# Kernel optimization log

Measured on AMD Instinct MI355X. Metric: run time of the kernel, lower is better.

The kernel has to match this reference:

```python
import jax, jax.numpy as jnp
import numpy as np
from jax import lax

IOU_THRESHOLD = 0.5
TOP = 1000


def setup_inputs() -> dict:
    key = jax.random.key(0)
    k1, k2, k3, k4, k5 = jax.random.split(key, 5)
    B, P = 16, 20000
    # valid (x1, y1, x2, y2) boxes on an ~800x800 image
    x1 = jax.random.uniform(k1, (B, P)) * 800.0
    y1 = jax.random.uniform(k2, (B, P)) * 800.0
    w = jax.random.uniform(k3, (B, P)) * 200.0 + 1.0
    h = jax.random.uniform(k4, (B, P)) * 200.0 + 1.0
    reg = jnp.stack([x1, y1, x1 + w, y1 + h], axis=-1)  # [B, P, 4]
    cls = jax.random.normal(k5, (B, P))                  # [B, P]
    return {"reg": reg, "cls": cls}


def _pairwise_iou(boxes):
    """boxes: [B, N, 4] (x1,y1,x2,y2) -> IoU [B, N, N]."""
    a = boxes[:, :, None, :]  # [B, N, 1, 4]
    b = boxes[:, None, :, :]  # [B, 1, N, 4]
    xx1 = jnp.maximum(a[..., 0], b[..., 0])
    yy1 = jnp.maximum(a[..., 1], b[..., 1])
    xx2 = jnp.minimum(a[..., 2], b[..., 2])
    yy2 = jnp.minimum(a[..., 3], b[..., 3])
    inter = jnp.clip(xx2 - xx1, 0.0) * jnp.clip(yy2 - yy1, 0.0)
    area_a = (a[..., 2] - a[..., 0]) * (a[..., 3] - a[..., 1])
    area_b = (b[..., 2] - b[..., 0]) * (b[..., 3] - b[..., 1])
    return inter / (area_a + area_b - inter)


def reference(reg, cls):
    B = cls.shape[0]
    # sort by confidence descending, gather boxes, keep top
    order = jnp.argsort(-cls, axis=1)                      # [B, P]
    sorted_cls = jnp.take_along_axis(cls, order, axis=1)[:, :TOP]            # [B, N]
    sorted_reg = jnp.take_along_axis(reg, order[:, :, None], axis=1)[:, :TOP]  # [B, N, 4]
    N = sorted_cls.shape[1]

    iou = _pairwise_iou(sorted_reg)                        # [B, N, N]

    # sequential greedy suppression: if box i still kept, drop boxes with IoU>=thr
    def body(mask, i):
        keep_i = mask[:, i]                                # [B]
        tmp = iou[:, i, :] < IOU_THRESHOLD                 # [B, N]
        upd = (mask & tmp).at[:, i].set(True)
        new_mask = jnp.where(keep_i[:, None], upd, mask)
        return new_mask, None

    mask0 = jnp.ones((B, N), dtype=bool)
    mask, _ = lax.scan(body, mask0, jnp.arange(N))

    out_reg = jnp.where(mask[:, :, None], sorted_reg, 0.0)
    out_cls = jnp.where(mask, sorted_cls, 0.0)
    return out_reg, out_cls
```

## Files before the change

kernel.cpp:

```cpp
#include <hip/hip_runtime.h>
#include <stdint.h>

#define BATCH 16
#define NPTS  20000
#define TOPK  1000
#define NKPT  20
#define NBIN  2048
#define NCOPY 4
#define CANDCAP 2048

__device__ __forceinline__ uint32_t key_desc(float f) {
    uint32_t u = __float_as_uint(f);
    uint32_t m = (u & 0x80000000u) ? ~u : (u | 0x80000000u);
    return ~m;
}

__device__ __forceinline__ float key_undo(uint32_t k) {
    uint32_t m = ~k;
    uint32_t u = (m & 0x80000000u) ? (m & 0x7FFFFFFFu) : ~m;
    return __uint_as_float(u);
}

__device__ __forceinline__ void hist_scan_find(
    uint32_t (*wh)[NBIN], uint32_t* wsum, uint32_t* wpre,
    int* sh_T, int* sh_r, int* sh_binc,
    int tid, int wave, int lane, uint32_t r)
{
    uint32_t m0 = 0, m1 = 0;
    #pragma unroll
    for (int cpy = 0; cpy < NCOPY; ++cpy) { m0 += wh[cpy][2*tid]; m1 += wh[cpy][2*tid+1]; }
    uint32_t s = m0 + m1, x = s;
    #pragma unroll
    for (int d = 1; d < 64; d <<= 1) { uint32_t t = __shfl_up(x, d); if (lane >= d) x += t; }
    if (lane == 63) wsum[wave] = x;
    __syncthreads();
    if (wave == 0 && lane < 16) {
        uint32_t v = wsum[lane], y = v;
        #pragma unroll
        for (int d = 1; d < 16; d <<= 1) { uint32_t t = __shfl_up(y, d); if (lane >= d) y += t; }
        wpre[lane] = y - v;
    }
    __syncthreads();
    uint32_t e = wpre[wave] + (x - s);
    if (r >= e && r < e + s) {
        if (r < e + m0) { *sh_T = 2*tid;     *sh_r = (int)(r - e);      *sh_binc = (int)m0; }
        else            { *sh_T = 2*tid + 1; *sh_r = (int)(r - e - m0); *sh_binc = (int)m1; }
    }
}

__device__ __forceinline__ void push64(bool pred, uint64_t val, int* cntr,
                                       uint64_t* list, int lane) {
    uint64_t mask = __ballot(pred);
    if (mask) {
        int first = __ffsll((long long)mask) - 1;
        int base = 0;
        if (lane == first) base = atomicAdd(cntr, (int)__popcll(mask));
        base = __shfl(base, first);
        if (pred) {
            int off = (int)__popcll(mask & ((1ull << lane) - 1ull));
            list[base + off] = val;
        }
    }
}

__device__ __forceinline__ void wave_select(const uint64_t* lst, int n, int r,
                                            uint64_t* out, int wave, int lane) {
    if (wave == 0) {
        uint64_t my = (lane < n) ? lst[lane] : ~0ull;
        int rank = 0;
        for (int i = 0; i < n; ++i) { uint64_t o = __shfl(my, i); if (o < my) rank++; }
        if (lane < n && rank == r) *out = my;
    }
}

__device__ uint64_t bit_search(const uint32_t* klds, uint64_t known, uint64_t kmask,
                               int startbit, uint32_t r, int* sh_c,
                               int tid, int lane) {
    for (int bit = startbit; bit >= 0; --bit) {
        if (tid == 0) *sh_c = 0;
        __syncthreads();
        uint32_t local = 0;
        #pragma unroll
        for (int j = 0; j < NKPT; ++j) {
            int p = tid + j * 1024;
            if (p < NPTS) {
                uint64_t k64 = ((uint64_t)klds[p] << 32) | (uint32_t)p;
                if ((k64 & kmask) == known && !((k64 >> bit) & 1ull)) local++;
            }
        }
        #pragma unroll
        for (int d = 1; d < 64; d <<= 1) local += __shfl_xor(local, d);
        if (lane == 0 && local) atomicAdd(sh_c, (int)local);
        __syncthreads();
        uint32_t c0 = (uint32_t)*sh_c;
        if (r >= c0) { known |= 1ull << bit; r -= c0; }
        kmask |= 1ull << bit;
        __syncthreads();
    }
    return known;
}

__global__ __launch_bounds__(1024) void topk_kernel(
    const float* __restrict__ reg, const float* __restrict__ cls,
    float4* __restrict__ ws_boxes, float* __restrict__ ws_cls)
{
    __shared__ uint32_t klds[NPTS];
    __shared__ uint32_t whist[NCOPY][NBIN];
    __shared__ uint32_t wsum[16], wpre[16];
    __shared__ int      sh_T, sh_r, sh_binc, sh_cnt;
    __shared__ uint64_t sh_kthkey;
    __shared__ uint64_t cand[CANDCAP];
    __shared__ uint64_t cand2[64];
    __shared__ uint64_t sel[1024];

    const int b = blockIdx.x, tid = threadIdx.x;
    const int wave = tid >> 6, lane = tid & 63;
    const float* c = cls + (size_t)b * NPTS;

    #pragma unroll
    for (int i = 0; i < NCOPY * NBIN / 1024; ++i) ((uint32_t*)whist)[tid + i * 1024] = 0;
    #pragma unroll
    for (int j = 0; j < NKPT; ++j) {
        int p = tid + j * 1024;
        if (p < NPTS) klds[p] = key_desc(c[p]);
    }
    __syncthreads();

    #pragma unroll
    for (int j = 0; j < NKPT; ++j) {
        int p = tid + j * 1024;
        if (p < NPTS) atomicAdd(&whist[wave >> 2][klds[p] >> 21], 1u);
    }
    __syncthreads();
    hist_scan_find(whist, wsum, wpre, &sh_T, &sh_r, &sh_binc, tid, wave, lane, TOPK - 1);
    __syncthreads();
    const int T1 = sh_T; int r = sh_r; const int cnt1 = sh_binc;
    uint64_t known = (uint64_t)(uint32_t)T1 << 53;

    if (cnt1 <= 64) {
        if (tid == 0) sh_cnt = 0;
        __syncthreads();
        #pragma unroll
        for (int j = 0; j < NKPT; ++j) {
            int p = tid + j * 1024;
            uint32_t k = (p < NPTS) ? klds[p] : 0xFFFFFFFFu;
            push64(p < NPTS && (k >> 21) == (uint32_t)T1,
                   ((uint64_t)k << 32) | (uint32_t)p, &sh_cnt, cand2, lane);
        }
        __syncthreads();
        wave_select(cand2, cnt1, r, &sh_kthkey, wave, lane);
        __syncthreads();
    } else if (cnt1 <= CANDCAP) {
        if (tid == 0) sh_cnt = 0;
        __syncthreads();
        #pragma unroll
        for (int j = 0; j < NKPT; ++j) {
            int p = tid + j * 1024;
            uint32_t k = (p < NPTS) ? klds[p] : 0xFFFFFFFFu;
            push64(p < NPTS && (k >> 21) == (uint32_t)T1,
                   ((uint64_t)k << 32) | (uint32_t)p, &sh_cnt, cand, lane);
        }
        __syncthreads();
        #pragma unroll
        for (int i = 0; i < NCOPY * NBIN / 1024; ++i) ((uint32_t*)whist)[tid + i * 1024] = 0;
        __syncthreads();
        for (int i = tid; i < cnt1; i += 1024)
            atomicAdd(&whist[wave >> 2][(uint32_t)((cand[i] >> 42) & 2047)], 1u);
        __syncthreads();
        hist_scan_find(whist, wsum, wpre, &sh_T, &sh_r, &sh_binc, tid, wave, lane, (uint32_t)r);
        __syncthreads();
        const int T2 = sh_T; r = sh_r; const int cnt2 = sh_binc;
        known |= (uint64_t)(uint32_t)T2 << 42;
        if (cnt2 <= 64) {
            if (tid == 0) sh_cnt = 0;
            __syncthreads();
            for (int i = tid; i < cnt1; i += 1024)
                push64(((cand[i] >> 42) & 2047) == (uint64_t)(uint32_t)T2,
                       cand[i], &sh_cnt, cand2, lane);
            __syncthreads();
            wave_select(cand2, cnt2, r, &sh_kthkey, wave, lane);
            __syncthreads();
        } else {
            uint64_t kk = bit_search(klds, known, 0xFFFFFC0000000000ull, 41,
                                     (uint32_t)r, &sh_cnt, tid, lane);
            if (tid == 0) sh_kthkey = kk;
            __syncthreads();
        }
    } else {
        uint64_t kk = bit_search(klds, known, 0xFFE0000000000000ull, 52,
                                 (uint32_t)r, &sh_cnt, tid, lane);
        if (tid == 0) sh_kthkey = kk;
        __syncthreads();
    }
    const uint64_t kthkey = sh_kthkey;

    if (tid == 0) sh_cnt = 0;
    sel[tid] = ~0ull;
    __syncthreads();
    #pragma unroll
    for (int j = 0; j < NKPT; ++j) {
        int p = tid + j * 1024;
        uint64_t key = (p < NPTS) ? (((uint64_t)klds[p] << 32) | (uint32_t)p) : ~0ull;
        push64(key <= kthkey, key, &sh_cnt, sel, lane);
    }
    __syncthreads();

    uint64_t v = sel[tid];
    for (int k = 2; k <= 1024; k <<= 1) {
        for (int j = k >> 1; j >= 64; j >>= 1) {
            __syncthreads();
            sel[tid] = v;
            __syncthreads();
            uint64_t o = sel[tid ^ j];
            bool upper = (tid & j) != 0;
            bool asc   = (tid & k) == 0;
            v = (upper == asc) ? (v > o ? v : o) : (v < o ? v : o);
        }
        int j0 = (k >> 1) < 64 ? (k >> 1) : 32;
        for (int j = j0; j >= 1; j >>= 1) {
            uint64_t o = __shfl_xor(v, j);
            bool upper = (tid & j) != 0;
            bool asc   = (tid & k) == 0;
            v = (upper == asc) ? (v > o ? v : o) : (v < o ? v : o);
        }
    }

    if (tid < TOPK) {
        int p = (int)(v & 0xFFFFFFFFull);
        ws_boxes[b * TOPK + tid] = ((const float4*)reg)[(size_t)b * NPTS + p];
        ws_cls[b * TOPK + tid] = key_undo((uint32_t)(v >> 32));
    }
}

__global__ __launch_bounds__(256) void iou_kernel(
    const float4* __restrict__ ws_boxes, uint32_t* __restrict__ suppT)
{
    __shared__ float4 boxes[TOPK];
    __shared__ float  areas[TOPK];
    const int b     = blockIdx.y;
    const int chunk = blockIdx.x;
    const int tid   = threadIdx.x;
    for (int j = tid; j < TOPK; j += 256) {
        float4 v = ws_boxes[b * TOPK + j];
        boxes[j] = v;
        areas[j] = (v.z - v.x) * (v.w - v.y);
    }
    __syncthreads();

    const int lane = tid & 63;
    const int wave = tid >> 6;
    const int rbeg = chunk * 63;
    const int rend = (rbeg + 63 < TOPK) ? (rbeg + 63) : TOPK;
    uint32_t* t = suppT + (size_t)b * 32 * 1024;

    for (int i = rbeg + wave; i < rend; i += 4) {
        float4 a = boxes[i];
        float areaA = areas[i];
        uint64_t mine = 0;
        #pragma unroll
        for (int w = 0; w < 16; ++w) {
            int col = (w << 6) | lane;
            bool sup = false;
            if (col < TOPK) {
                float4 bb = boxes[col];
                float xx1 = fmaxf(a.x, bb.x);
                float yy1 = fmaxf(a.y, bb.y);
                float xx2 = fminf(a.z, bb.z);
                float yy2 = fminf(a.w, bb.w);
                float iw = fmaxf(xx2 - xx1, 0.0f);
                float ih = fmaxf(yy2 - yy1, 0.0f);
                float inter = iw * ih;
                float areaB = areas[col];
                float iou = inter / (areaA + areaB - inter);
                sup = (iou >= 0.5f);
            }
            uint64_t m = __ballot(sup);
            if (lane == w) mine = m;
        }
        if (lane < 16) {
            t[(2 * lane + 0) * 1024 + i] = (uint32_t)(mine & 0xFFFFFFFFull);
            t[(2 * lane + 1) * 1024 + i] = (uint32_t)(mine >> 32);
        }
    }
}

__global__ __launch_bounds__(64) void sweep_kernel(
    const uint32_t* __restrict__ suppT, const float4* __restrict__ ws_boxes,
    const float* __restrict__ ws_cls, float* __restrict__ out)
{
    const int b    = blockIdx.x;
    const int lane = threadIdx.x;
    const int myw  = lane & 31;
    const uint32_t* base = suppT + (size_t)b * 32 * 1024;

    uint32_t remv = 0, keptw = 0;
    uint4 dgA[8], clA[8], dgB[8], clB[8];

#define LOADG(W, DG, CL) { \
    const uint4* dp_ = (const uint4*)(base + (W) * 1024 + (W) * 32); \
    const uint4* cp_ = (const uint4*)(base + myw * 1024 + (W) * 32); \
    _Pragma("unroll") \
    for (int k_ = 0; k_ < 8; ++k_) { DG[k_] = dp_[k_]; CL[k_] = cp_[k_]; } }

#define STEP(D, C, BBIT) { \
    uint32_t live_ = (((~cur) >> (BBIT)) & 1u) & (uint32_t)((BBIT) < nb); \
    uint32_t msk_ = (uint32_t)0 - live_; \
    kmask |= (live_ << (BBIT)); \
    cur  |= (D) & msk_; \
    acc  |= (C) & msk_; }

#define PROC(W, DG, CL) { \
    const int nb = ((W) == 31) ? (TOPK - 31 * 32) : 32; \
    uint32_t cur = __shfl(remv, (W)); \
    uint32_t kmask = 0, acc = 0; \
    _Pragma("unroll") \
    for (int k_ = 0; k_ < 8; ++k_) { \
        STEP(DG[k_].x, CL[k_].x, 4 * k_ + 0); \
        STEP(DG[k_].y, CL[k_].y, 4 * k_ + 1); \
        STEP(DG[k_].z, CL[k_].z, 4 * k_ + 2); \
        STEP(DG[k_].w, CL[k_].w, 4 * k_ + 3); \
    } \
    remv |= acc; \
    if (myw == (W)) keptw = kmask; }

    LOADG(0, dgA, clA);
    #pragma unroll 1
    for (int w2 = 0; w2 < 16; ++w2) {
        const int wE = 2 * w2, wO = 2 * w2 + 1;
        LOADG(wO, dgB, clB);
        PROC(wE, dgA, clA);
        if (wO + 1 < 32) LOADG(wO + 1, dgA, clA);
        PROC(wO, dgB, clB);
    }

    __shared__ uint32_t skept[32];
    if (lane < 32) skept[lane] = keptw;
    __syncthreads();

    const float4* bx = ws_boxes + (size_t)b * TOPK;
    const float*  bc = ws_cls + (size_t)b * TOPK;
    float4* outr = (float4*)out + (size_t)b * TOPK;
    float*  outc = out + (size_t)BATCH * TOPK * 4 + (size_t)b * TOPK;
    for (int j = lane; j < TOPK; j += 64) {
        uint32_t keep = (skept[j >> 5] >> (j & 31)) & 1u;
        float4 v = bx[j];
        float cv = bc[j];
        outr[j] = keep ? v : make_float4(0.f, 0.f, 0.f, 0.f);
        outc[j] = keep ? cv : 0.0f;
    }
#undef LOADG
#undef STEP
#undef PROC
}

extern "C" void kernel_launch(void* const* d_in, const int* in_sizes, int n_in,
                              void* d_out, int out_size, void* d_ws, size_t ws_size,
                              hipStream_t stream) {
    (void)in_sizes; (void)n_in; (void)out_size; (void)ws_size;
    const float* reg = (const float*)d_in[0];
    const float* cls = (const float*)d_in[1];
    float* out = (float*)d_out;
    char* ws = (char*)d_ws;

    float4*   ws_boxes = (float4*)ws;
    float*    ws_cls   = (float*)(ws + 256000);
    uint32_t* suppT    = (uint32_t*)(ws + 320000);

    topk_kernel<<<dim3(BATCH), dim3(1024), 0, stream>>>(reg, cls, ws_boxes, ws_cls);
    iou_kernel<<<dim3(16, BATCH), dim3(256), 0, stream>>>(ws_boxes, suppT);
    sweep_kernel<<<dim3(BATCH), dim3(64), 0, stream>>>(suppT, ws_boxes, ws_cls, out);
}
```

Measured before the change: 74.24 us.

## Use single-level 4096-bin top-k select, rank-count ordering, upper-triangle IoU

The top-k selection now uses one 4096-bin histogram pass instead of a two-level 2048-bin refinement with a candidate buffer. Inputs whose threshold bin holds more than 64 entries fall back to a bit search. The 1024-element bitonic sort, with its many block barriers, is replaced by having each thread count how many selected keys are smaller than its own and scatter to that rank. The IoU kernel now computes only the upper-triangular 64-column words for each row and interleaves rows across blocks to balance the triangular work. Costs: the rank count does 1024 shared reads per thread, and the larger histogram uses more LDS and takes longer to clear and scan.

```diff
diff --git a/kernel.cpp b/kernel.cpp
--- a/kernel.cpp
+++ b/kernel.cpp
@@ -5,9 +5,8 @@
 #define NPTS  20000
 #define TOPK  1000
 #define NKPT  20
-#define NBIN  2048
+#define NBIN  4096
 #define NCOPY 4
-#define CANDCAP 2048
 
 __device__ __forceinline__ uint32_t key_desc(float f) {
     uint32_t u = __float_as_uint(f);
@@ -19,33 +18,6 @@
     uint32_t m = ~k;
     uint32_t u = (m & 0x80000000u) ? (m & 0x7FFFFFFFu) : ~m;
     return __uint_as_float(u);
-}
-
-__device__ __forceinline__ void hist_scan_find(
-    uint32_t (*wh)[NBIN], uint32_t* wsum, uint32_t* wpre,
-    int* sh_T, int* sh_r, int* sh_binc,
-    int tid, int wave, int lane, uint32_t r)
-{
-    uint32_t m0 = 0, m1 = 0;
-    #pragma unroll
-    for (int cpy = 0; cpy < NCOPY; ++cpy) { m0 += wh[cpy][2*tid]; m1 += wh[cpy][2*tid+1]; }
-    uint32_t s = m0 + m1, x = s;
-    #pragma unroll
-    for (int d = 1; d < 64; d <<= 1) { uint32_t t = __shfl_up(x, d); if (lane >= d) x += t; }
-    if (lane == 63) wsum[wave] = x;
-    __syncthreads();
-    if (wave == 0 && lane < 16) {
-        uint32_t v = wsum[lane], y = v;
-        #pragma unroll
-        for (int d = 1; d < 16; d <<= 1) { uint32_t t = __shfl_up(y, d); if (lane >= d) y += t; }
-        wpre[lane] = y - v;
-    }
-    __syncthreads();
-    uint32_t e = wpre[wave] + (x - s);
-    if (r >= e && r < e + s) {
-        if (r < e + m0) { *sh_T = 2*tid;     *sh_r = (int)(r - e);      *sh_binc = (int)m0; }
-        else            { *sh_T = 2*tid + 1; *sh_r = (int)(r - e - m0); *sh_binc = (int)m1; }
-    }
 }
 
 __device__ __forceinline__ void push64(bool pred, uint64_t val, int* cntr,
@@ -106,10 +78,9 @@
 {
     __shared__ uint32_t klds[NPTS];
     __shared__ uint32_t whist[NCOPY][NBIN];
-    __shared__ uint32_t wsum[16], wpre[16];
-    __shared__ int      sh_T, sh_r, sh_binc, sh_cnt;
+    __shared__ uint32_t wsum[16], wpre16[16];
+    __shared__ int      sh_T, sh_r, sh_binc, sh_cnt, sh_c;
     __shared__ uint64_t sh_kthkey;
-    __shared__ uint64_t cand[CANDCAP];
     __shared__ uint64_t cand2[64];
     __shared__ uint64_t sel[1024];
 
@@ -129,13 +100,42 @@
     #pragma unroll
     for (int j = 0; j < NKPT; ++j) {
         int p = tid + j * 1024;
-        if (p < NPTS) atomicAdd(&whist[wave >> 2][klds[p] >> 21], 1u);
-    }
-    __syncthreads();
-    hist_scan_find(whist, wsum, wpre, &sh_T, &sh_r, &sh_binc, tid, wave, lane, TOPK - 1);
-    __syncthreads();
-    const int T1 = sh_T; int r = sh_r; const int cnt1 = sh_binc;
-    uint64_t known = (uint64_t)(uint32_t)T1 << 53;
+        if (p < NPTS) atomicAdd(&whist[wave >> 2][klds[p] >> 20], 1u);
+    }
+    __syncthreads();
+
+    {
+        uint32_t m0 = 0, m1 = 0, m2 = 0, m3 = 0;
+        #pragma unroll
+        for (int cpy = 0; cpy < NCOPY; ++cpy) {
+            m0 += whist[cpy][4 * tid + 0]; m1 += whist[cpy][4 * tid + 1];
+            m2 += whist[cpy][4 * tid + 2]; m3 += whist[cpy][4 * tid + 3];
+        }
+        uint32_t s = m0 + m1 + m2 + m3, x = s;
+        #pragma unroll
+        for (int d = 1; d < 64; d <<= 1) { uint32_t t = __shfl_up(x, d); if (lane >= d) x += t; }
+        if (lane == 63) wsum[wave] = x;
+        __syncthreads();
+        if (wave == 0 && lane < 16) {
+            uint32_t v = wsum[lane], y = v;
+            #pragma unroll
+            for (int d = 1; d < 16; d <<= 1) { uint32_t t = __shfl_up(y, d); if (lane >= d) y += t; }
+            wpre16[lane] = y - v;
+        }
+        __syncthreads();
+        uint32_t E = wpre16[wave] + (x - s);
+        uint32_t r9 = TOPK - 1;
+        if (r9 >= E && r9 < E + s) {
+            uint32_t rr = r9 - E;
+            if      (rr < m0)           { sh_T = 4*tid + 0; sh_r = (int)rr;            sh_binc = (int)m0; }
+            else if (rr < m0+m1)        { sh_T = 4*tid + 1; sh_r = (int)(rr-m0);       sh_binc = (int)m1; }
+            else if (rr < m0+m1+m2)     { sh_T = 4*tid + 2; sh_r = (int)(rr-m0-m1);    sh_binc = (int)m2; }
+            else                        { sh_T = 4*tid + 3; sh_r = (int)(rr-m0-m1-m2); sh_binc = (int)m3; }
+        }
+    }
+    __syncthreads();
+    const uint32_t T1 = (uint32_t)sh_T;
+    const int r = sh_r, cnt1 = sh_binc;
 
     if (cnt1 <= 64) {
         if (tid == 0) sh_cnt = 0;
@@ -144,54 +144,17 @@
         for (int j = 0; j < NKPT; ++j) {
             int p = tid + j * 1024;
             uint32_t k = (p < NPTS) ? klds[p] : 0xFFFFFFFFu;
-            push64(p < NPTS && (k >> 21) == (uint32_t)T1,
+            push64(p < NPTS && (k >> 20) == T1,
                    ((uint64_t)k << 32) | (uint32_t)p, &sh_cnt, cand2, lane);
         }
         __syncthreads();
         wave_select(cand2, cnt1, r, &sh_kthkey, wave, lane);
-        __syncthreads();
-    } else if (cnt1 <= CANDCAP) {
-        if (tid == 0) sh_cnt = 0;
-        __syncthreads();
-        #pragma unroll
-        for (int j = 0; j < NKPT; ++j) {
-            int p = tid + j * 1024;
-            uint32_t k = (p < NPTS) ? klds[p] : 0xFFFFFFFFu;
-            push64(p < NPTS && (k >> 21) == (uint32_t)T1,
-                   ((uint64_t)k << 32) | (uint32_t)p, &sh_cnt, cand, lane);
-        }
-        __syncthreads();
-        #pragma unroll
-        for (int i = 0; i < NCOPY * NBIN / 1024; ++i) ((uint32_t*)whist)[tid + i * 1024] = 0;
-        __syncthreads();
-        for (int i = tid; i < cnt1; i += 1024)
-            atomicAdd(&whist[wave >> 2][(uint32_t)((cand[i] >> 42) & 2047)], 1u);
-        __syncthreads();
-        hist_scan_find(whist, wsum, wpre, &sh_T, &sh_r, &sh_binc, tid, wave, lane, (uint32_t)r);
-        __syncthreads();
-        const int T2 = sh_T; r = sh_r; const int cnt2 = sh_binc;
-        known |= (uint64_t)(uint32_t)T2 << 42;
-        if (cnt2 <= 64) {
-            if (tid == 0) sh_cnt = 0;
-            __syncthreads();
-            for (int i = tid; i < cnt1; i += 1024)
-                push64(((cand[i] >> 42) & 2047) == (uint64_t)(uint32_t)T2,
-                       cand[i], &sh_cnt, cand2, lane);
-            __syncthreads();
-            wave_select(cand2, cnt2, r, &sh_kthkey, wave, lane);
-            __syncthreads();
-        } else {
-            uint64_t kk = bit_search(klds, known, 0xFFFFFC0000000000ull, 41,
-                                     (uint32_t)r, &sh_cnt, tid, lane);
-            if (tid == 0) sh_kthkey = kk;
-            __syncthreads();
-        }
     } else {
-        uint64_t kk = bit_search(klds, known, 0xFFE0000000000000ull, 52,
-                                 (uint32_t)r, &sh_cnt, tid, lane);
+        uint64_t kk = bit_search(klds, (uint64_t)T1 << 52, 0xFFF0000000000000ull,
+                                 51, (uint32_t)r, &sh_c, tid, lane);
         if (tid == 0) sh_kthkey = kk;
-        __syncthreads();
-    }
+    }
+    __syncthreads();
     const uint64_t kthkey = sh_kthkey;
 
     if (tid == 0) sh_cnt = 0;
@@ -205,30 +168,14 @@
     }
     __syncthreads();
 
-    uint64_t v = sel[tid];
-    for (int k = 2; k <= 1024; k <<= 1) {
-        for (int j = k >> 1; j >= 64; j >>= 1) {
-            __syncthreads();
-            sel[tid] = v;
-            __syncthreads();
-            uint64_t o = sel[tid ^ j];
-            bool upper = (tid & j) != 0;
-            bool asc   = (tid & k) == 0;
-            v = (upper == asc) ? (v > o ? v : o) : (v < o ? v : o);
-        }
-        int j0 = (k >> 1) < 64 ? (k >> 1) : 32;
-        for (int j = j0; j >= 1; j >>= 1) {
-            uint64_t o = __shfl_xor(v, j);
-            bool upper = (tid & j) != 0;
-            bool asc   = (tid & k) == 0;
-            v = (upper == asc) ? (v > o ? v : o) : (v < o ? v : o);
-        }
-    }
-
-    if (tid < TOPK) {
-        int p = (int)(v & 0xFFFFFFFFull);
-        ws_boxes[b * TOPK + tid] = ((const float4*)reg)[(size_t)b * NPTS + p];
-        ws_cls[b * TOPK + tid] = key_undo((uint32_t)(v >> 32));
+    uint64_t e = sel[tid];
+    int rk = 0;
+    #pragma unroll 4
+    for (int m2 = 0; m2 < 1024; ++m2) rk += (sel[m2] < e) ? 1 : 0;
+    if (e != ~0ull) {
+        int p = (int)(e & 0xFFFFFFFFull);
+        ws_boxes[b * TOPK + rk] = ((const float4*)reg)[(size_t)b * NPTS + p];
+        ws_cls[b * TOPK + rk] = key_undo((uint32_t)(e >> 32));
     }
 }
 
@@ -237,29 +184,28 @@
 {
     __shared__ float4 boxes[TOPK];
     __shared__ float  areas[TOPK];
-    const int b     = blockIdx.y;
-    const int chunk = blockIdx.x;
-    const int tid   = threadIdx.x;
-    for (int j = tid; j < TOPK; j += 256) {
-        float4 v = ws_boxes[b * TOPK + j];
-        boxes[j] = v;
-        areas[j] = (v.z - v.x) * (v.w - v.y);
+    const int b   = blockIdx.y;
+    const int j   = blockIdx.x;
+    const int tid = threadIdx.x;
+    for (int i = tid; i < TOPK; i += 256) {
+        float4 v = ws_boxes[b * TOPK + i];
+        boxes[i] = v;
+        areas[i] = (v.z - v.x) * (v.w - v.y);
     }
     __syncthreads();
 
     const int lane = tid & 63;
     const int wave = tid >> 6;
-    const int rbeg = chunk * 63;
-    const int rend = (rbeg + 63 < TOPK) ? (rbeg + 63) : TOPK;
     uint32_t* t = suppT + (size_t)b * 32 * 1024;
 
-    for (int i = rbeg + wave; i < rend; i += 4) {
+    for (int k = wave; ; k += 4) {
+        const int i = j + (k << 4);
+        if (i >= TOPK) break;
         float4 a = boxes[i];
         float areaA = areas[i];
         uint64_t mine = 0;
-        #pragma unroll
-        for (int w = 0; w < 16; ++w) {
-            int col = (w << 6) | lane;
+        for (int w2 = i >> 6; w2 < 16; ++w2) {
+            int col = (w2 << 6) | lane;
             bool sup = false;
             if (col < TOPK) {
                 float4 bb = boxes[col];
@@ -270,12 +216,11 @@
                 float iw = fmaxf(xx2 - xx1, 0.0f);
                 float ih = fmaxf(yy2 - yy1, 0.0f);
                 float inter = iw * ih;
-                float areaB = areas[col];
-                float iou = inter / (areaA + areaB - inter);
+                float iou = inter / (areaA + areas[col] - inter);
                 sup = (iou >= 0.5f);
             }
             uint64_t m = __ballot(sup);
-            if (lane == w) mine = m;
+            if (lane == w2) mine = m;
         }
         if (lane < 16) {
             t[(2 * lane + 0) * 1024 + i] = (uint32_t)(mine & 0xFFFFFFFFull);
@@ -341,12 +286,12 @@
     const float*  bc = ws_cls + (size_t)b * TOPK;
     float4* outr = (float4*)out + (size_t)b * TOPK;
     float*  outc = out + (size_t)BATCH * TOPK * 4 + (size_t)b * TOPK;
-    for (int j = lane; j < TOPK; j += 64) {
-        uint32_t keep = (skept[j >> 5] >> (j & 31)) & 1u;
-        float4 v = bx[j];
-        float cv = bc[j];
-        outr[j] = keep ? v : make_float4(0.f, 0.f, 0.f, 0.f);
-        outc[j] = keep ? cv : 0.0f;
+    for (int i = lane; i < TOPK; i += 64) {
+        uint32_t keep = (skept[i >> 5] >> (i & 31)) & 1u;
+        float4 v = bx[i];
+        float cv = bc[i];
+        outr[i] = keep ? v : make_float4(0.f, 0.f, 0.f, 0.f);
+        outc[i] = keep ? cv : 0.0f;
     }
 #undef LOADG
 #undef STEP
```

After: 170.8 us. +130.0%, slower.
